# Kernel tuning notes

Measured on AMD Instinct MI355X. Metric: run time of the kernel, lower is better.

Reference implementation:

```python
import jax, jax.numpy as jnp
import numpy as np

N_NODES = 100000
N_EDGES = 600000
D_IN = 128
D_OUT = 128

def gcn_conv(x, src, dst, W, b, n):
    # PyG GCNConv: h = X W; out_i = sum_j norm_ij * h_j + b, with self-loops and
    # symmetric normalization norm_ij = deg_i^{-1/2} deg_j^{-1/2}.
    deg = jax.ops.segment_sum(jnp.ones_like(dst, dtype=x.dtype), dst, num_segments=n)
    dinv = jnp.where(deg > 0, jax.lax.rsqrt(deg), 0.0)
    norm = dinv[src] * dinv[dst]            # [E]
    h = x @ W                                # [N, D_out]
    msg = h[src] * norm[:, None]             # gather + scale, [E, D_out]
    out = jax.ops.segment_sum(msg, dst, num_segments=n)
    return out + b

def setup_inputs() -> dict:
    key = jax.random.key(0)
    ks = jax.random.split(key, 8)
    x = jax.random.normal(ks[0], (N_NODES, D_IN), dtype=jnp.float32)
    edge_index = jax.random.randint(ks[1], (2, N_EDGES), 0, N_NODES, dtype=jnp.int64)
    s = (1.0 / np.sqrt(D_IN)).astype(np.float32) if isinstance(np.sqrt(D_IN), np.ndarray) else np.float32(1.0 / np.sqrt(D_IN))
    W1 = jax.random.normal(ks[2], (D_IN, D_OUT), dtype=jnp.float32) * s
    b1 = jnp.zeros((D_OUT,), dtype=jnp.float32)
    W2 = jax.random.normal(ks[3], (D_OUT, D_OUT), dtype=jnp.float32) * np.float32(1.0 / np.sqrt(D_OUT))
    b2 = jnp.zeros((D_OUT,), dtype=jnp.float32)
    Wfc = jax.random.normal(ks[4], (D_IN, D_OUT), dtype=jnp.float32) * s
    bfc = jnp.zeros((D_OUT,), dtype=jnp.float32)
    return {"x": x, "edge_index": edge_index, "W1": W1, "b1": b1,
            "W2": W2, "b2": b2, "Wfc": Wfc, "bfc": bfc}

def reference(x, edge_index, W1, b1, W2, b2, Wfc, bfc):
    n = x.shape[0]
    loop = jnp.arange(n, dtype=edge_index.dtype)
    src = jnp.concatenate([edge_index[0], loop])  # add self-loops
    dst = jnp.concatenate([edge_index[1], loop])
    res = x @ Wfc + bfc                           # linear residual branch
    h = jax.nn.relu(gcn_conv(x, src, dst, W1, b1, n))
    h = jax.nn.relu(gcn_conv(h, src, dst, W2, b2, n))
    return h + res
```

## Files before the change

### kernel.cpp

```cpp
#include <hip/hip_runtime.h>
#include <hip/hip_bf16.h>

#define D 128

typedef __bf16 bf16x8 __attribute__((ext_vector_type(8)));
typedef float f32x16 __attribute__((ext_vector_type(16)));

union U16 { uint4 u; bf16x8 v; };

static __device__ __forceinline__ unsigned short f2bf(float f) {
    unsigned u = __float_as_uint(f);
    unsigned r = (u + 0x7fffu + ((u >> 16) & 1u)) >> 16;
    return (unsigned short)r;
}
static __device__ __forceinline__ float bf2f(unsigned short s) {
    return __uint_as_float(((unsigned)s) << 16);
}
static __device__ __forceinline__ float u2f_lo(unsigned x) { return __uint_as_float(x << 16); }
static __device__ __forceinline__ float u2f_hi(unsigned x) { return __uint_as_float(x & 0xffff0000u); }

__global__ __launch_bounds__(256) void k_prep(
        const float* __restrict__ W1, const float* __restrict__ W2, const float* __restrict__ Wf,
        unsigned short* __restrict__ W1h, unsigned short* __restrict__ W1l,
        unsigned short* __restrict__ W2h, unsigned short* __restrict__ W2l,
        unsigned short* __restrict__ Wfh, unsigned short* __restrict__ Wfl,
        int* __restrict__ cnt, int n) {
    int idx = blockIdx.x * 256 + threadIdx.x;
    if (idx < 3 * 16384) {
        int which = idx >> 14;
        int local = idx & 16383;
        int k = local >> 7, c = local & 127;
        const float* W = (which == 0) ? W1 : (which == 1) ? W2 : Wf;
        unsigned short* Wh = (which == 0) ? W1h : (which == 1) ? W2h : Wfh;
        unsigned short* Wl = (which == 0) ? W1l : (which == 1) ? W2l : Wfl;
        float v = W[k * 128 + c];
        unsigned short h = f2bf(v);
        unsigned short l = f2bf(v - bf2f(h));
        Wh[c * 128 + k] = h;
        Wl[c * 128 + k] = l;
    }
    if (idx < n) cnt[idx] = 0;
}


__global__ __launch_bounds__(256) void k_hist(const int* __restrict__ dst,
                                              int* __restrict__ cnt, int e) {
    int i = blockIdx.x * 256 + threadIdx.x;
    if (i < e) atomicAdd(&cnt[dst[i]], 1);
}

#define SCAN_CHUNK 1024

__global__ __launch_bounds__(256) void k_scan_local(const int* __restrict__ cnt,
                                                    int* __restrict__ ptr,
                                                    int* __restrict__ sums, int n) {
    __shared__ int tsum[256];
    const int t = threadIdx.x;
    const int base = blockIdx.x * SCAN_CHUNK + t * 4;
    int v[4]; int s = 0;
    #pragma unroll
    for (int i = 0; i < 4; ++i) {
        int idx = base + i;
        v[i] = (idx < n) ? cnt[idx] : 0;
        s += v[i];
    }
    tsum[t] = s;
    __syncthreads();
    for (int off = 1; off < 256; off <<= 1) {
        int x = (t >= off) ? tsum[t - off] : 0;
        __syncthreads();
        tsum[t] += x;
        __syncthreads();
    }
    int run = (t > 0) ? tsum[t - 1] : 0;
    if (t == 255) sums[blockIdx.x] = tsum[255];
    #pragma unroll
    for (int i = 0; i < 4; ++i) {
        int idx = base + i;
        if (idx < n) ptr[idx] = run;
        run += v[i];
    }
}

__global__ __launch_bounds__(256) void k_scan_sums(int* __restrict__ sums, int nChunks) {
    __shared__ int ls[256];
    const int t = threadIdx.x;
    ls[t] = (t < nChunks) ? sums[t] : 0;
    __syncthreads();
    for (int off = 1; off < 256; off <<= 1) {
        int x = (t >= off) ? ls[t - off] : 0;
        __syncthreads();
        ls[t] += x;
        __syncthreads();
    }
    if (t < nChunks) sums[t] = (t > 0) ? ls[t - 1] : 0;
}

__global__ __launch_bounds__(256) void k_scan_add(int* __restrict__ ptr,
                                                  const int* __restrict__ sums,
                                                  int* __restrict__ cnt,
                                                  float* __restrict__ dinv,
                                                  int n, int e) {
    int i = blockIdx.x * 256 + threadIdx.x;
    if (i < n) {
        ptr[i] += sums[i >> 10];
        dinv[i] = rsqrtf((float)(1 + cnt[i]));
        cnt[i] = 0;
    }
    if (i == 0) ptr[n] = e;
}

__global__ __launch_bounds__(256) void k_fill(const int* __restrict__ src,
                                              const int* __restrict__ dst,
                                              const int* __restrict__ ptr,
                                              int* __restrict__ fill,
                                              int* __restrict__ csr_src, int e) {
    int i = blockIdx.x * 256 + threadIdx.x;
    if (i < e) {
        int d = dst[i];
        int slot = ptr[d] + atomicAdd(&fill[d], 1);
        csr_src[slot] = src[i];
    }
}

#define APAD 136

__global__ __launch_bounds__(256, 4) void k_gemm_rr(
        const float* __restrict__ A,
        const unsigned short* __restrict__ Bh, const unsigned short* __restrict__ Bl,
        const float* __restrict__ bias,
        unsigned short* __restrict__ outb,
        float* __restrict__ outf,
        int M, int nTiles) {
    __shared__ __align__(16) unsigned short As[2][32][APAD];

    const int tid = threadIdx.x;
    const int wave = tid >> 6;
    const int lane = tid & 63;
    const int l31 = lane & 31;
    const int quad8 = (lane >> 5) * 8;
    const int col = wave * 32 + l31;

    U16 bh[8], bl[8];
    #pragma unroll
    for (int ks = 0; ks < 8; ++ks) {
        const size_t bo = (size_t)col * D + ks * 16 + quad8;
        bh[ks].u = *(const uint4*)(Bh + bo);
        bl[ks].u = *(const uint4*)(Bl + bo);
    }
    const float bv = (bias != nullptr) ? bias[col] : 0.f;

    for (int t = blockIdx.x; t < nTiles; t += gridDim.x) {
        const int row0 = t * 32;

        #pragma unroll
        for (int i = 0; i < 4; ++i) {
            int f = tid + i * 256;
            int r = f >> 5, c4 = (f & 31) * 4;
            int rg = row0 + r; if (rg >= M) rg = M - 1;
            float4 v = *(const float4*)(A + (size_t)rg * D + c4);
            ushort4 hq, lq;
            hq.x = f2bf(v.x); hq.y = f2bf(v.y); hq.z = f2bf(v.z); hq.w = f2bf(v.w);
            lq.x = f2bf(v.x - bf2f(hq.x)); lq.y = f2bf(v.y - bf2f(hq.y));
            lq.z = f2bf(v.z - bf2f(hq.z)); lq.w = f2bf(v.w - bf2f(hq.w));
            *(ushort4*)&As[0][r][c4] = hq;
            *(ushort4*)&As[1][r][c4] = lq;
        }
        __syncthreads();

        f32x16 acc;
        #pragma unroll
        for (int r = 0; r < 16; ++r) acc[r] = 0.f;

        #pragma unroll
        for (int ks = 0; ks < 8; ++ks) {
            U16 ah, al;
            ah.u = *(const uint4*)&As[0][l31][ks * 16 + quad8];
            al.u = *(const uint4*)&As[1][l31][ks * 16 + quad8];
            acc = __builtin_amdgcn_mfma_f32_32x32x16_bf16(ah.v, bh[ks].v, acc, 0, 0, 0);
            acc = __builtin_amdgcn_mfma_f32_32x32x16_bf16(ah.v, bl[ks].v, acc, 0, 0, 0);
            acc = __builtin_amdgcn_mfma_f32_32x32x16_bf16(al.v, bh[ks].v, acc, 0, 0, 0);
        }
        __syncthreads();

        #pragma unroll
        for (int reg = 0; reg < 16; ++reg) {
            const int r = (reg & 3) + 8 * (reg >> 2) + 4 * (lane >> 5);
            const int rg = row0 + r;
            if (rg < M) {
                if (outb) outb[(size_t)rg * D + col] = f2bf(acc[reg]);
                else      outf[(size_t)rg * D + col] = acc[reg] + bv;
            }
        }
    }
}

__global__ __launch_bounds__(256, 4) void k_gemm_rr_bf(
        const unsigned short* __restrict__ A,
        const unsigned short* __restrict__ Bh, const unsigned short* __restrict__ Bl,
        unsigned short* __restrict__ outb,
        int M, int nTiles) {
    __shared__ __align__(16) unsigned short As[32][APAD];

    const int tid = threadIdx.x;
    const int wave = tid >> 6;
    const int lane = tid & 63;
    const int l31 = lane & 31;
    const int quad8 = (lane >> 5) * 8;
    const int col = wave * 32 + l31;

    U16 bh[8], bl[8];
    #pragma unroll
    for (int ks = 0; ks < 8; ++ks) {
        const size_t bo = (size_t)col * D + ks * 16 + quad8;
        bh[ks].u = *(const uint4*)(Bh + bo);
        bl[ks].u = *(const uint4*)(Bl + bo);
    }

    for (int t = blockIdx.x; t < nTiles; t += gridDim.x) {
        const int row0 = t * 32;

        #pragma unroll
        for (int i = 0; i < 2; ++i) {
            int f = tid + i * 256;
            int r = f >> 4, c8 = (f & 15) * 8;
            int rg = row0 + r; if (rg >= M) rg = M - 1;
            *(uint4*)&As[r][c8] = *(const uint4*)(A + (size_t)rg * D + c8);
        }
        __syncthreads();

        f32x16 acc;
        #pragma unroll
        for (int r = 0; r < 16; ++r) acc[r] = 0.f;

        #pragma unroll
        for (int ks = 0; ks < 8; ++ks) {
            U16 ah;
            ah.u = *(const uint4*)&As[l31][ks * 16 + quad8];
            acc = __builtin_amdgcn_mfma_f32_32x32x16_bf16(ah.v, bh[ks].v, acc, 0, 0, 0);
            acc = __builtin_amdgcn_mfma_f32_32x32x16_bf16(ah.v, bl[ks].v, acc, 0, 0, 0);
        }
        __syncthreads();

        #pragma unroll
        for (int reg = 0; reg < 16; ++reg) {
            const int r = (reg & 3) + 8 * (reg >> 2) + 4 * (lane >> 5);
            const int rg = row0 + r;
            if (rg < M) outb[(size_t)rg * D + col] = f2bf(acc[reg]);
        }
    }
}

__global__ __launch_bounds__(256) void k_gather_bf(const int* __restrict__ ptr,
                                                   const int* __restrict__ csr_src,
                                                   const float* __restrict__ dinv,
                                                   const unsigned short* __restrict__ h,
                                                   const float* __restrict__ bias,
                                                   const float* __restrict__ res,
                                                   float* __restrict__ outf,
                                                   unsigned short* __restrict__ outb,
                                                   int N) {
    const int g = threadIdx.x >> 5;
    const int lane = threadIdx.x & 31;
    const int i = blockIdx.x * 8 + g;
    if (i >= N) return;

    const int p0 = ptr[i];
    const int p1 = ptr[i + 1];
    const float di = dinv[i];

    float a0 = 0.f, a1 = 0.f, a2 = 0.f, a3 = 0.f;
    int j = p0;
    for (; j + 4 <= p1; j += 4) {
        const int s0 = csr_src[j + 0];
        const int s1 = csr_src[j + 1];
        const int s2 = csr_src[j + 2];
        const int s3 = csr_src[j + 3];
        const float c0 = dinv[s0], c1 = dinv[s1], c2 = dinv[s2], c3 = dinv[s3];
        const uint2 u0 = *(const uint2*)(h + (size_t)s0 * D + lane * 4);
        const uint2 u1 = *(const uint2*)(h + (size_t)s1 * D + lane * 4);
        const uint2 u2 = *(const uint2*)(h + (size_t)s2 * D + lane * 4);
        const uint2 u3 = *(const uint2*)(h + (size_t)s3 * D + lane * 4);
        a0 = fmaf(c0, u2f_lo(u0.x), a0); a1 = fmaf(c0, u2f_hi(u0.x), a1);
        a2 = fmaf(c0, u2f_lo(u0.y), a2); a3 = fmaf(c0, u2f_hi(u0.y), a3);
        a0 = fmaf(c1, u2f_lo(u1.x), a0); a1 = fmaf(c1, u2f_hi(u1.x), a1);
        a2 = fmaf(c1, u2f_lo(u1.y), a2); a3 = fmaf(c1, u2f_hi(u1.y), a3);
        a0 = fmaf(c2, u2f_lo(u2.x), a0); a1 = fmaf(c2, u2f_hi(u2.x), a1);
        a2 = fmaf(c2, u2f_lo(u2.y), a2); a3 = fmaf(c2, u2f_hi(u2.y), a3);
        a0 = fmaf(c3, u2f_lo(u3.x), a0); a1 = fmaf(c3, u2f_hi(u3.x), a1);
        a2 = fmaf(c3, u2f_lo(u3.y), a2); a3 = fmaf(c3, u2f_hi(u3.y), a3);
    }
    for (; j < p1; ++j) {
        const int s = csr_src[j];
        const float c = dinv[s];
        const uint2 u = *(const uint2*)(h + (size_t)s * D + lane * 4);
        a0 = fmaf(c, u2f_lo(u.x), a0);
        a1 = fmaf(c, u2f_hi(u.x), a1);
        a2 = fmaf(c, u2f_lo(u.y), a2);
        a3 = fmaf(c, u2f_hi(u.y), a3);
    }

    const uint2 us = *(const uint2*)(h + (size_t)i * D + lane * 4);
    const float4 bv = *(const float4*)(bias + lane * 4);
    const float self = di * di;
    float o0 = fmaxf(di * a0 + self * u2f_lo(us.x) + bv.x, 0.0f);
    float o1 = fmaxf(di * a1 + self * u2f_hi(us.x) + bv.y, 0.0f);
    float o2 = fmaxf(di * a2 + self * u2f_lo(us.y) + bv.z, 0.0f);
    float o3 = fmaxf(di * a3 + self * u2f_hi(us.y) + bv.w, 0.0f);
    if (outb) {
        ushort4 q = {f2bf(o0), f2bf(o1), f2bf(o2), f2bf(o3)};
        *(ushort4*)(outb + (size_t)i * D + lane * 4) = q;
    } else {
        if (res) {
            const float4 rv = *(const float4*)(res + (size_t)i * D + lane * 4);
            o0 += rv.x; o1 += rv.y; o2 += rv.z; o3 += rv.w;
        }
        float4 o = {o0, o1, o2, o3};
        *(float4*)(outf + (size_t)i * D + lane * 4) = o;
    }
}


extern "C" void kernel_launch(void* const* d_in, const int* in_sizes, int n_in,
                              void* d_out, int out_size, void* d_ws, size_t ws_size,
                              hipStream_t stream) {
    const int N = in_sizes[0] / D;
    const int E = in_sizes[1] / 2;

    const float* x   = (const float*)d_in[0];
    const int*   ei  = (const int*)d_in[1];
    const int*   src = ei;
    const int*   dst = ei + E;
    const float* W1  = (const float*)d_in[2];
    const float* b1  = (const float*)d_in[3];
    const float* W2  = (const float*)d_in[4];
    const float* b2  = (const float*)d_in[5];
    const float* Wfc = (const float*)d_in[6];
    const float* bfc = (const float*)d_in[7];
    float* out = (float*)d_out;

    char* ws = (char*)d_ws;
    size_t off = 0;
    auto alloc = [&](size_t bytes) { char* p = ws + off; off += (bytes + 255) & ~(size_t)255; return p; };
    float* dinv    = (float*)alloc((size_t)N * 4);
    int*   cnt     = (int*)  alloc((size_t)N * 4);
    int*   ptr     = (int*)  alloc((size_t)(N + 1) * 4);
    int*   sums    = (int*)  alloc(256 * 4);
    int*   csr_src = (int*)  alloc((size_t)E * 4);
    unsigned short* W1h = (unsigned short*)alloc(128 * 128 * 2);
    unsigned short* W1l = (unsigned short*)alloc(128 * 128 * 2);
    unsigned short* W2h = (unsigned short*)alloc(128 * 128 * 2);
    unsigned short* W2l = (unsigned short*)alloc(128 * 128 * 2);
    unsigned short* Wfh = (unsigned short*)alloc(128 * 128 * 2);
    unsigned short* Wfl = (unsigned short*)alloc(128 * 128 * 2);
    unsigned short* h    = (unsigned short*)alloc((size_t)N * D * 2);
    unsigned short* hb16 = (unsigned short*)alloc((size_t)N * D * 2);

    const int nBlk    = (N + 255) / 256;
    const int eBlk    = (E + 255) / 256;
    const int aBlk    = (N + 7) / 8;
    const int nChunks = (N + SCAN_CHUNK - 1) / SCAN_CHUNK;
    const int nTiles  = (N + 31) / 32;
    const int gBlk    = nTiles < 1024 ? nTiles : 1024;
    const int pBlk    = (nBlk > 192) ? nBlk : 192;

    k_prep<<<pBlk, 256, 0, stream>>>(W1, W2, Wfc, W1h, W1l, W2h, W2l, Wfh, Wfl, cnt, N);

    k_hist<<<eBlk, 256, 0, stream>>>(dst, cnt, E);
    k_scan_local<<<nChunks, 256, 0, stream>>>(cnt, ptr, sums, N);
    k_scan_sums<<<1, 256, 0, stream>>>(sums, nChunks);
    k_scan_add<<<nBlk, 256, 0, stream>>>(ptr, sums, cnt, dinv, N, E);
    k_fill<<<eBlk, 256, 0, stream>>>(src, dst, ptr, cnt, csr_src, E);

    k_gemm_rr<<<gBlk, 256, 0, stream>>>(x, W1h, W1l, nullptr, h, nullptr, N, nTiles);
    k_gemm_rr<<<gBlk, 256, 0, stream>>>(x, Wfh, Wfl, bfc, nullptr, out, N, nTiles);

    k_gather_bf<<<aBlk, 256, 0, stream>>>(ptr, csr_src, dinv, h, b1, nullptr, nullptr, hb16, N);

    k_gemm_rr_bf<<<gBlk, 256, 0, stream>>>(hb16, W2h, W2l, h, N, nTiles);

    k_gather_bf<<<aBlk, 256, 0, stream>>>(ptr, csr_src, dinv, h, b2, out, out, nullptr, N);
}
```

Baseline: 304.6 us.

## Fuse dual input GEMMs and fuse layer-1 aggregation into layer-2 GEMM

Merges the two x-side GEMMs (x@W1 and x@Wfc) into one kernel, so x is read and split into hi/lo bf16 parts only once. The residual branch now uses a cheaper two-term split with no low part of Wfc. The layer-1 gather/normalize/ReLU is fused into the layer-2 GEMM, which builds each 32-row A tile in shared memory via an atomic work counter. This removes the hb16 intermediate round trip and a kernel launch, but lowers occupancy (launch bounds 2 and 3) and puts irregular gather latency in the GEMM kernel. The residual also loses a bit of precision.

```diff
diff --git a/kernel.cpp b/kernel.cpp
--- a/kernel.cpp
+++ b/kernel.cpp
@@ -23,7 +23,7 @@
         const float* __restrict__ W1, const float* __restrict__ W2, const float* __restrict__ Wf,
         unsigned short* __restrict__ W1h, unsigned short* __restrict__ W1l,
         unsigned short* __restrict__ W2h, unsigned short* __restrict__ W2l,
-        unsigned short* __restrict__ Wfh, unsigned short* __restrict__ Wfl,
+        unsigned short* __restrict__ Wfh,
         int* __restrict__ cnt, int n) {
     int idx = blockIdx.x * 256 + threadIdx.x;
     if (idx < 3 * 16384) {
@@ -31,13 +31,12 @@
         int local = idx & 16383;
         int k = local >> 7, c = local & 127;
         const float* W = (which == 0) ? W1 : (which == 1) ? W2 : Wf;
-        unsigned short* Wh = (which == 0) ? W1h : (which == 1) ? W2h : Wfh;
-        unsigned short* Wl = (which == 0) ? W1l : (which == 1) ? W2l : Wfl;
         float v = W[k * 128 + c];
         unsigned short h = f2bf(v);
         unsigned short l = f2bf(v - bf2f(h));
-        Wh[c * 128 + k] = h;
-        Wl[c * 128 + k] = l;
+        if (which == 0) { W1h[c * 128 + k] = h; W1l[c * 128 + k] = l; }
+        else if (which == 1) { W2h[c * 128 + k] = h; W2l[c * 128 + k] = l; }
+        else { Wfh[c * 128 + k] = h; }
     }
     if (idx < n) cnt[idx] = 0;
 }
@@ -125,12 +124,13 @@
 
 #define APAD 136
 
-__global__ __launch_bounds__(256, 4) void k_gemm_rr(
+__global__ __launch_bounds__(256, 2) void k_gemm_dual(
         const float* __restrict__ A,
-        const unsigned short* __restrict__ Bh, const unsigned short* __restrict__ Bl,
-        const float* __restrict__ bias,
-        unsigned short* __restrict__ outb,
-        float* __restrict__ outf,
+        const unsigned short* __restrict__ B1h, const unsigned short* __restrict__ B1l,
+        const unsigned short* __restrict__ B2h,
+        const float* __restrict__ bias2,
+        unsigned short* __restrict__ out1,
+        float* __restrict__ out2,
         int M, int nTiles) {
     __shared__ __align__(16) unsigned short As[2][32][APAD];
 
@@ -141,14 +141,15 @@
     const int quad8 = (lane >> 5) * 8;
     const int col = wave * 32 + l31;
 
-    U16 bh[8], bl[8];
+    U16 bh1[8], bl1[8], bh2[8];
     #pragma unroll
     for (int ks = 0; ks < 8; ++ks) {
         const size_t bo = (size_t)col * D + ks * 16 + quad8;
-        bh[ks].u = *(const uint4*)(Bh + bo);
-        bl[ks].u = *(const uint4*)(Bl + bo);
-    }
-    const float bv = (bias != nullptr) ? bias[col] : 0.f;
+        bh1[ks].u = *(const uint4*)(B1h + bo);
+        bl1[ks].u = *(const uint4*)(B1l + bo);
+        bh2[ks].u = *(const uint4*)(B2h + bo);
+    }
+    const float bv = bias2[col];
 
     for (int t = blockIdx.x; t < nTiles; t += gridDim.x) {
         const int row0 = t * 32;
@@ -168,18 +169,20 @@
         }
         __syncthreads();
 
-        f32x16 acc;
-        #pragma unroll
-        for (int r = 0; r < 16; ++r) acc[r] = 0.f;
+        f32x16 acc1, acc2;
+        #pragma unroll
+        for (int r = 0; r < 16; ++r) { acc1[r] = 0.f; acc2[r] = 0.f; }
 
         #pragma unroll
         for (int ks = 0; ks < 8; ++ks) {
             U16 ah, al;
             ah.u = *(const uint4*)&As[0][l31][ks * 16 + quad8];
             al.u = *(const uint4*)&As[1][l31][ks * 16 + quad8];
-            acc = __builtin_amdgcn_mfma_f32_32x32x16_bf16(ah.v, bh[ks].v, acc, 0, 0, 0);
-            acc = __builtin_amdgcn_mfma_f32_32x32x16_bf16(ah.v, bl[ks].v, acc, 0, 0, 0);
-            acc = __builtin_amdgcn_mfma_f32_32x32x16_bf16(al.v, bh[ks].v, acc, 0, 0, 0);
+            acc1 = __builtin_amdgcn_mfma_f32_32x32x16_bf16(ah.v, bh1[ks].v, acc1, 0, 0, 0);
+            acc1 = __builtin_amdgcn_mfma_f32_32x32x16_bf16(ah.v, bl1[ks].v, acc1, 0, 0, 0);
+            acc1 = __builtin_amdgcn_mfma_f32_32x32x16_bf16(al.v, bh1[ks].v, acc1, 0, 0, 0);
+            acc2 = __builtin_amdgcn_mfma_f32_32x32x16_bf16(ah.v, bh2[ks].v, acc2, 0, 0, 0);
+            acc2 = __builtin_amdgcn_mfma_f32_32x32x16_bf16(al.v, bh2[ks].v, acc2, 0, 0, 0);
         }
         __syncthreads();
 
@@ -188,19 +191,23 @@
             const int r = (reg & 3) + 8 * (reg >> 2) + 4 * (lane >> 5);
             const int rg = row0 + r;
             if (rg < M) {
-                if (outb) outb[(size_t)rg * D + col] = f2bf(acc[reg]);
-                else      outf[(size_t)rg * D + col] = acc[reg] + bv;
+                out1[(size_t)rg * D + col] = f2bf(acc1[reg]);
+                out2[(size_t)rg * D + col] = acc2[reg] + bv;
             }
         }
     }
 }
 
-__global__ __launch_bounds__(256, 4) void k_gemm_rr_bf(
-        const unsigned short* __restrict__ A,
+__global__ __launch_bounds__(256, 3) void k_agg_gemm(
+        const int* __restrict__ ptr, const int* __restrict__ csr_src,
+        const float* __restrict__ dinv,
+        const unsigned short* __restrict__ h,
+        const float* __restrict__ bias,
         const unsigned short* __restrict__ Bh, const unsigned short* __restrict__ Bl,
-        unsigned short* __restrict__ outb,
-        int M, int nTiles) {
+        unsigned short* __restrict__ outh,
+        int N, int nTiles) {
     __shared__ __align__(16) unsigned short As[32][APAD];
+    __shared__ int ctr;
 
     const int tid = threadIdx.x;
     const int wave = tid >> 6;
@@ -208,6 +215,7 @@
     const int l31 = lane & 31;
     const int quad8 = (lane >> 5) * 8;
     const int col = wave * 32 + l31;
+    const int glane = tid & 31;
 
     U16 bh[8], bl[8];
     #pragma unroll
@@ -216,16 +224,63 @@
         bh[ks].u = *(const uint4*)(Bh + bo);
         bl[ks].u = *(const uint4*)(Bl + bo);
     }
+    const float4 bvec = *(const float4*)(bias + glane * 4);
 
     for (int t = blockIdx.x; t < nTiles; t += gridDim.x) {
         const int row0 = t * 32;
-
-        #pragma unroll
-        for (int i = 0; i < 2; ++i) {
-            int f = tid + i * 256;
-            int r = f >> 4, c8 = (f & 15) * 8;
-            int rg = row0 + r; if (rg >= M) rg = M - 1;
-            *(uint4*)&As[r][c8] = *(const uint4*)(A + (size_t)rg * D + c8);
+        if (tid == 0) ctr = 0;
+        __syncthreads();
+
+        while (true) {
+            int q = 0;
+            if (glane == 0) q = atomicAdd(&ctr, 1);
+            q = __shfl(q, (int)(tid & 32), 64);
+            if (q >= 32) break;
+            int i = row0 + q; if (i >= N) i = N - 1;
+
+            const int p0 = ptr[i];
+            const int p1 = ptr[i + 1];
+            const float di = dinv[i];
+
+            float a0 = 0.f, a1 = 0.f, a2 = 0.f, a3 = 0.f;
+            int j = p0;
+            for (; j + 4 <= p1; j += 4) {
+                const int s0 = csr_src[j + 0];
+                const int s1 = csr_src[j + 1];
+                const int s2 = csr_src[j + 2];
+                const int s3 = csr_src[j + 3];
+                const float c0 = dinv[s0], c1 = dinv[s1], c2 = dinv[s2], c3 = dinv[s3];
+                const uint2 u0 = *(const uint2*)(h + (size_t)s0 * D + glane * 4);
+                const uint2 u1 = *(const uint2*)(h + (size_t)s1 * D + glane * 4);
+                const uint2 u2 = *(const uint2*)(h + (size_t)s2 * D + glane * 4);
+                const uint2 u3 = *(const uint2*)(h + (size_t)s3 * D + glane * 4);
+                a0 = fmaf(c0, u2f_lo(u0.x), a0); a1 = fmaf(c0, u2f_hi(u0.x), a1);
+                a2 = fmaf(c0, u2f_lo(u0.y), a2); a3 = fmaf(c0, u2f_hi(u0.y), a3);
+                a0 = fmaf(c1, u2f_lo(u1.x), a0); a1 = fmaf(c1, u2f_hi(u1.x), a1);
+                a2 = fmaf(c1, u2f_lo(u1.y), a2); a3 = fmaf(c1, u2f_hi(u1.y), a3);
+                a0 = fmaf(c2, u2f_lo(u2.x), a0); a1 = fmaf(c2, u2f_hi(u2.x), a1);
+                a2 = fmaf(c2, u2f_lo(u2.y), a2); a3 = fmaf(c2, u2f_hi(u2.y), a3);
+                a0 = fmaf(c3, u2f_lo(u3.x), a0); a1 = fmaf(c3, u2f_hi(u3.x), a1);
+                a2 = fmaf(c3, u2f_lo(u3.y), a2); a3 = fmaf(c3, u2f_hi(u3.y), a3);
+            }
+            for (; j < p1; ++j) {
+                const int s = csr_src[j];
+                const float c = dinv[s];
+                const uint2 u = *(const uint2*)(h + (size_t)s * D + glane * 4);
+                a0 = fmaf(c, u2f_lo(u.x), a0);
+                a1 = fmaf(c, u2f_hi(u.x), a1);
+                a2 = fmaf(c, u2f_lo(u.y), a2);
+                a3 = fmaf(c, u2f_hi(u.y), a3);
+            }
+
+            const uint2 us = *(const uint2*)(h + (size_t)i * D + glane * 4);
+            const float self = di * di;
+            float o0 = fmaxf(di * a0 + self * u2f_lo(us.x) + bvec.x, 0.0f);
+            float o1 = fmaxf(di * a1 + self * u2f_hi(us.x) + bvec.y, 0.0f);
+            float o2 = fmaxf(di * a2 + self * u2f_lo(us.y) + bvec.z, 0.0f);
+            float o3 = fmaxf(di * a3 + self * u2f_hi(us.y) + bvec.w, 0.0f);
+            ushort4 qv = {f2bf(o0), f2bf(o1), f2bf(o2), f2bf(o3)};
+            *(ushort4*)&As[q][glane * 4] = qv;
         }
         __syncthreads();
 
@@ -240,14 +295,14 @@
             acc = __builtin_amdgcn_mfma_f32_32x32x16_bf16(ah.v, bh[ks].v, acc, 0, 0, 0);
             acc = __builtin_amdgcn_mfma_f32_32x32x16_bf16(ah.v, bl[ks].v, acc, 0, 0, 0);
         }
-        __syncthreads();
 
         #pragma unroll
         for (int reg = 0; reg < 16; ++reg) {
             const int r = (reg & 3) + 8 * (reg >> 2) + 4 * (lane >> 5);
             const int rg = row0 + r;
-            if (rg < M) outb[(size_t)rg * D + col] = f2bf(acc[reg]);
-        }
+            if (rg < N) outh[(size_t)rg * D + col] = f2bf(acc[reg]);
+        }
+        __syncthreads();
     }
 }
 
@@ -258,7 +313,6 @@
                                                    const float* __restrict__ bias,
                                                    const float* __restrict__ res,
                                                    float* __restrict__ outf,
-                                                   unsigned short* __restrict__ outb,
                                                    int N) {
     const int g = threadIdx.x >> 5;
     const int lane = threadIdx.x & 31;
@@ -307,17 +361,9 @@
     float o1 = fmaxf(di * a1 + self * u2f_hi(us.x) + bv.y, 0.0f);
     float o2 = fmaxf(di * a2 + self * u2f_lo(us.y) + bv.z, 0.0f);
     float o3 = fmaxf(di * a3 + self * u2f_hi(us.y) + bv.w, 0.0f);
-    if (outb) {
-        ushort4 q = {f2bf(o0), f2bf(o1), f2bf(o2), f2bf(o3)};
-        *(ushort4*)(outb + (size_t)i * D + lane * 4) = q;
-    } else {
-        if (res) {
-            const float4 rv = *(const float4*)(res + (size_t)i * D + lane * 4);
-            o0 += rv.x; o1 += rv.y; o2 += rv.z; o3 += rv.w;
-        }
-        float4 o = {o0, o1, o2, o3};
-        *(float4*)(outf + (size_t)i * D + lane * 4) = o;
-    }
+    const float4 rv = *(const float4*)(res + (size_t)i * D + lane * 4);
+    float4 o = {o0 + rv.x, o1 + rv.y, o2 + rv.z, o3 + rv.w};
+    *(float4*)(outf + (size_t)i * D + lane * 4) = o;
 }
 
 
@@ -352,19 +398,19 @@
     unsigned short* W2h = (unsigned short*)alloc(128 * 128 * 2);
     unsigned short* W2l = (unsigned short*)alloc(128 * 128 * 2);
     unsigned short* Wfh = (unsigned short*)alloc(128 * 128 * 2);
-    unsigned short* Wfl = (unsigned short*)alloc(128 * 128 * 2);
-    unsigned short* h    = (unsigned short*)alloc((size_t)N * D * 2);
-    unsigned short* hb16 = (unsigned short*)alloc((size_t)N * D * 2);
+    unsigned short* h1  = (unsigned short*)alloc((size_t)N * D * 2);
+    unsigned short* h2  = (unsigned short*)alloc((size_t)N * D * 2);
 
     const int nBlk    = (N + 255) / 256;
     const int eBlk    = (E + 255) / 256;
     const int aBlk    = (N + 7) / 8;
     const int nChunks = (N + SCAN_CHUNK - 1) / SCAN_CHUNK;
     const int nTiles  = (N + 31) / 32;
-    const int gBlk    = nTiles < 1024 ? nTiles : 1024;
+    const int gDual   = nTiles < 512 ? nTiles : 512;
+    const int gAgg    = nTiles < 768 ? nTiles : 768;
     const int pBlk    = (nBlk > 192) ? nBlk : 192;
 
-    k_prep<<<pBlk, 256, 0, stream>>>(W1, W2, Wfc, W1h, W1l, W2h, W2l, Wfh, Wfl, cnt, N);
+    k_prep<<<pBlk, 256, 0, stream>>>(W1, W2, Wfc, W1h, W1l, W2h, W2l, Wfh, cnt, N);
 
     k_hist<<<eBlk, 256, 0, stream>>>(dst, cnt, E);
     k_scan_local<<<nChunks, 256, 0, stream>>>(cnt, ptr, sums, N);
@@ -372,12 +418,9 @@
     k_scan_add<<<nBlk, 256, 0, stream>>>(ptr, sums, cnt, dinv, N, E);
     k_fill<<<eBlk, 256, 0, stream>>>(src, dst, ptr, cnt, csr_src, E);
 
-    k_gemm_rr<<<gBlk, 256, 0, stream>>>(x, W1h, W1l, nullptr, h, nullptr, N, nTiles);
-    k_gemm_rr<<<gBlk, 256, 0, stream>>>(x, Wfh, Wfl, bfc, nullptr, out, N, nTiles);
-
-    k_gather_bf<<<aBlk, 256, 0, stream>>>(ptr, csr_src, dinv, h, b1, nullptr, nullptr, hb16, N);
-
-    k_gemm_rr_bf<<<gBlk, 256, 0, stream>>>(hb16, W2h, W2l, h, N, nTiles);
-
-    k_gather_bf<<<aBlk, 256, 0, stream>>>(ptr, csr_src, dinv, h, b2, out, out, nullptr, N);
-}
+    k_gemm_dual<<<gDual, 256, 0, stream>>>(x, W1h, W1l, Wfh, bfc, h1, out, N, nTiles);
+
+    k_agg_gemm<<<gAgg, 256, 0, stream>>>(ptr, csr_src, dinv, h1, b1, W2h, W2l, h2, N, nTiles);
+
+    k_gather_bf<<<aBlk, 256, 0, stream>>>(ptr, csr_src, dinv, h2, b2, out, out, N);
+}
```

After: 312.4 us. +2.6%, slower.
